# Kernel optimization log

Hardware: AMD Instinct MI355X
Metric: run time of the kernel (lower is better)

The kernel has to match this reference:

```python
import jax, jax.numpy as jnp
import numpy as np

B, T, C = 4, 2048, 1024
H = 16
DH = C // H  # 64


def setup_inputs() -> dict:
    key = jax.random.key(0)
    ks = jax.random.split(key, 10)
    s_in = 1.0 / np.sqrt(C)
    x = jax.random.normal(ks[0], (B, T, C), dtype=jnp.float32)
    # stacked per-head projection weights: [H, C, DH]
    Wq = jax.random.normal(ks[1], (H, C, DH), dtype=jnp.float32) * s_in
    bq = jnp.zeros((H, DH), dtype=jnp.float32)
    Wk = jax.random.normal(ks[2], (H, C, DH), dtype=jnp.float32) * s_in
    bk = jnp.zeros((H, DH), dtype=jnp.float32)
    Wv = jax.random.normal(ks[3], (H, C, DH), dtype=jnp.float32) * s_in
    bv = jnp.zeros((H, DH), dtype=jnp.float32)
    Wo = jax.random.normal(ks[4], (C, C), dtype=jnp.float32) * s_in
    bo = jnp.zeros((C,), dtype=jnp.float32)
    return {"x": x, "Wq": Wq, "bq": bq, "Wk": Wk, "bk": bk,
            "Wv": Wv, "bv": bv, "Wo": Wo, "bo": bo}


def reference(x, Wq, bq, Wk, bk, Wv, bv, Wo, bo):
    # per-head projections: (B,T,C) x (H,C,DH) -> (B,H,T,DH)
    q = jnp.einsum('btc,hcd->bhtd', x, Wq) + bq[None, :, None, :]
    k = jnp.einsum('btc,hcd->bhtd', x, Wk) + bk[None, :, None, :]
    v = jnp.einsum('btc,hcd->bhtd', x, Wv) + bv[None, :, None, :]
    # scores scaled by C**-0.5 (C = full input embedding dim, as in source)
    scale = jnp.float32(C) ** -0.5
    scores = jnp.einsum('bhtd,bhsd->bhts', q, k) * scale  # (B,H,T,T)
    causal = jnp.tril(jnp.ones((T, T), dtype=bool))
    scores = jnp.where(causal, scores, -jnp.inf)
    attn = jax.nn.softmax(scores, axis=-1)
    out = jnp.einsum('bhts,bhsd->bhtd', attn, v)  # (B,H,T,DH)
    out = out.transpose(0, 2, 1, 3).reshape(B, T, C)  # concat heads
    return out @ Wo + bo
```

## Files before the change

### kernel.cpp

```cpp
#include <hip/hip_runtime.h>
#include <hip/hip_bf16.h>

#define TDIM 2048
#define BDIM 4
#define CDIM 1024
#define HDIM 16
#define DH   64

typedef __hip_bfloat16 bf16;
typedef __attribute__((ext_vector_type(8))) short bf16x8;
typedef __attribute__((ext_vector_type(4))) short bf16x4;
typedef __attribute__((ext_vector_type(4))) float f32x4;

__device__ __forceinline__ void async_ld16(const bf16* g, bf16* l) {
    __builtin_amdgcn_global_load_lds(
        (const __attribute__((address_space(1))) unsigned int*)g,
        (__attribute__((address_space(3))) unsigned int*)l, 16, 0, 0);
}

__device__ __forceinline__ unsigned short bf16bits(float x) {
    bf16 b = __float2bfloat16(x);
    return *(unsigned short*)&b;
}

__device__ __forceinline__ float fast_exp2(float x) {
#if __has_builtin(__builtin_amdgcn_exp2f)
    return __builtin_amdgcn_exp2f(x);
#else
    return exp2f(x);
#endif
}

__device__ __forceinline__ f32x4 mfma_16x16x16_bf16(bf16x4 a, bf16x4 b, f32x4 c) {
#if __has_builtin(__builtin_amdgcn_mfma_f32_16x16x16_bf16)
    return __builtin_amdgcn_mfma_f32_16x16x16_bf16(a, b, c, 0, 0, 0);
#elif __has_builtin(__builtin_amdgcn_mfma_f32_16x16x16bf16_1k)
    return __builtin_amdgcn_mfma_f32_16x16x16bf16_1k(a, b, c, 0, 0, 0);
#else
    asm volatile("v_mfma_f32_16x16x16_bf16 %0, %1, %2, %0"
                 : "+v"(c) : "v"(a), "v"(b));
    return c;
#endif
}

__global__ void convert_x4(const float4* __restrict__ src, ushort4* __restrict__ dst, int n4) {
    int i = blockIdx.x * blockDim.x + threadIdx.x;
    if (i >= n4) return;
    float4 v = src[i];
    ushort4 o;
    o.x = bf16bits(v.x); o.y = bf16bits(v.y);
    o.z = bf16bits(v.z); o.w = bf16bits(v.w);
    dst[i] = o;
}

__global__ void convert_biases(const float* __restrict__ b0, const float* __restrict__ b1,
                               const float* __restrict__ b2, const float* __restrict__ b3,
                               bf16* __restrict__ dst) {
    int i = blockIdx.x * blockDim.x + threadIdx.x;
    int which = i >> 10, j = i & 1023;
    const float* src = (which == 0) ? b0 : (which == 1) ? b1 : (which == 2) ? b2 : b3;
    dst[i] = __float2bfloat16(src[j]);
}

__global__ __launch_bounds__(256) void transpose_qkv_kernel(
    const float* __restrict__ Wq, const float* __restrict__ Wk, const float* __restrict__ Wv,
    bf16* __restrict__ WqT, bf16* __restrict__ WkT, bf16* __restrict__ WvT) {
    __shared__ float tile[64][65];
    const int which = blockIdx.z >> 4, h = blockIdx.z & 15;
    const float* W  = ((which == 0) ? Wq  : (which == 1) ? Wk  : Wv)  + (size_t)h * CDIM * DH;
    bf16*        WT = ((which == 0) ? WqT : (which == 1) ? WkT : WvT) + (size_t)h * CDIM * DH;
    const int c0 = blockIdx.x * 64;
    for (int it = 0; it < 16; it++) {
        int e = it * 256 + threadIdx.x;
        int r = e >> 6, col = e & 63;
        tile[r][col] = W[(size_t)(c0 + r) * DH + col];
    }
    __syncthreads();
    for (int it = 0; it < 16; it++) {
        int e = it * 256 + threadIdx.x;
        int r = e >> 6, col = e & 63;
        WT[(size_t)r * CDIM + c0 + col] = __float2bfloat16(tile[col][r]);
    }
}

__global__ __launch_bounds__(256) void transpose_wo_kernel(
    const float* __restrict__ W, bf16* __restrict__ WT) {
    __shared__ float tile[64][65];
    const int c0 = blockIdx.x * 64, d0 = blockIdx.y * 64;
    for (int it = 0; it < 16; it++) {
        int e = it * 256 + threadIdx.x;
        int r = e >> 6, col = e & 63;
        tile[r][col] = W[(size_t)(c0 + r) * CDIM + d0 + col];
    }
    __syncthreads();
    for (int it = 0; it < 16; it++) {
        int e = it * 256 + threadIdx.x;
        int r = e >> 6, col = e & 63;
        WT[(size_t)(d0 + r) * CDIM + c0 + col] = __float2bfloat16(tile[col][r]);
    }
}

__global__ __launch_bounds__(256) void transpose_v_kernel(
    const bf16* __restrict__ V, bf16* __restrict__ Vt) {
    __shared__ unsigned short tile[64][65];
    const int bh = blockIdx.y, t0 = blockIdx.x * 64;
    const unsigned short* Vp  = (const unsigned short*)V + ((size_t)bh * TDIM + t0) * DH;
    unsigned short*       Vtp = (unsigned short*)Vt + (size_t)bh * DH * TDIM;
    for (int it = 0; it < 16; it++) {
        int e = it * 256 + threadIdx.x;
        int r = e >> 6, c = e & 63;
        tile[r][c] = Vp[(size_t)r * DH + c];
    }
    __syncthreads();
    for (int it = 0; it < 16; it++) {
        int e = it * 256 + threadIdx.x;
        int r = e >> 6, c = e & 63;
        Vtp[(size_t)r * TDIM + t0 + c] = tile[c][r];
    }
}

__global__ __launch_bounds__(256) void proj_qkv_kernel(
    const bf16* __restrict__ X,
    const bf16* __restrict__ WqT, const bf16* __restrict__ WkT, const bf16* __restrict__ WvT,
    const bf16* __restrict__ bq,  const bf16* __restrict__ bk,  const bf16* __restrict__ bvv,
    bf16* __restrict__ Qo, bf16* __restrict__ Ko, bf16* __restrict__ Vo)
{
    const int z = blockIdx.z;
    const bf16* Bt   = (z == 0) ? WqT : (z == 1) ? WkT : WvT;
    const bf16* bias = (z == 0) ? bq  : (z == 1) ? bk  : bvv;

    __shared__ __align__(16) bf16 As[128 * 32];
    __shared__ __align__(16) bf16 Bs[128 * 32];

    const int tid  = threadIdx.x;
    const int lane = tid & 63;
    const int wave = tid >> 6;
    const int wr = wave >> 1, wc = wave & 1;
    const int l15 = lane & 15, quad = lane >> 4;

    const int blockM = blockIdx.y * 128;
    const int blockN = blockIdx.x * 128;

    f32x4 acc[4][4];
    for (int i = 0; i < 4; i++)
        for (int j = 0; j < 4; j++)
            acc[i][j] = (f32x4){0.f, 0.f, 0.f, 0.f};

    const int srow = lane >> 2, scol = (lane & 3) * 8;
    for (int k0 = 0; k0 < CDIM; k0 += 32) {
        for (int cc = 0; cc < 2; cc++) {
            int chunk = wave * 2 + cc;
            int row = chunk * 16 + srow;
            async_ld16(&X [(size_t)(blockM + row) * CDIM + k0 + scol], &As[chunk * 512]);
            async_ld16(&Bt[(size_t)(blockN + row) * CDIM + k0 + scol], &Bs[chunk * 512]);
        }
        __syncthreads();

        bf16x8 af[4], bfr[4];
        for (int mi = 0; mi < 4; mi++)
            af[mi] = *(const bf16x8*)&As[(wr * 64 + mi * 16 + l15) * 32 + quad * 8];
        for (int ni = 0; ni < 4; ni++)
            bfr[ni] = *(const bf16x8*)&Bs[(wc * 64 + ni * 16 + l15) * 32 + quad * 8];

        for (int mi = 0; mi < 4; mi++)
            for (int ni = 0; ni < 4; ni++)
                acc[mi][ni] = __builtin_amdgcn_mfma_f32_16x16x32_bf16(
                    af[mi], bfr[ni], acc[mi][ni], 0, 0, 0);
        __syncthreads();
    }

    for (int mi = 0; mi < 4; mi++) {
        int mbase = blockM + wr * 64 + mi * 16 + quad * 4;
        for (int ni = 0; ni < 4; ni++) {
            int n = blockN + wc * 64 + ni * 16 + l15;
            float bval = __bfloat162float(bias[n]);
            int h = n >> 6, d = n & 63;
            for (int r = 0; r < 4; r++) {
                int mm = mbase + r;
                int b = mm >> 11, t = mm & 2047;
                float val = acc[mi][ni][r] + bval;
                size_t idx = (((size_t)b * HDIM + h) * TDIM + t) * DH + d;
                if (z == 0)      Qo[idx] = __float2bfloat16(val * 0.045084439f);
                else if (z == 1) Ko[idx] = __float2bfloat16(val);
                else             Vo[idx] = __float2bfloat16(val);
            }
        }
    }
}

__global__ __launch_bounds__(256) void proj_out_kernel(
    const bf16* __restrict__ X, const bf16* __restrict__ Bt,
    const bf16* __restrict__ bias, float* __restrict__ Out)
{
    __shared__ __align__(16) bf16 As[128 * 32];
    __shared__ __align__(16) bf16 Bs[128 * 32];

    const int tid  = threadIdx.x;
    const int lane = tid & 63;
    const int wave = tid >> 6;
    const int wr = wave >> 1, wc = wave & 1;
    const int l15 = lane & 15, quad = lane >> 4;

    const int blockM = blockIdx.y * 128;
    const int blockN = blockIdx.x * 128;

    f32x4 acc[4][4];
    for (int i = 0; i < 4; i++)
        for (int j = 0; j < 4; j++)
            acc[i][j] = (f32x4){0.f, 0.f, 0.f, 0.f};

    const int srow = lane >> 2, scol = (lane & 3) * 8;
    for (int k0 = 0; k0 < CDIM; k0 += 32) {
        for (int cc = 0; cc < 2; cc++) {
            int chunk = wave * 2 + cc;
            int row = chunk * 16 + srow;
            async_ld16(&X [(size_t)(blockM + row) * CDIM + k0 + scol], &As[chunk * 512]);
            async_ld16(&Bt[(size_t)(blockN + row) * CDIM + k0 + scol], &Bs[chunk * 512]);
        }
        __syncthreads();

        bf16x8 af[4], bfr[4];
        for (int mi = 0; mi < 4; mi++)
            af[mi] = *(const bf16x8*)&As[(wr * 64 + mi * 16 + l15) * 32 + quad * 8];
        for (int ni = 0; ni < 4; ni++)
            bfr[ni] = *(const bf16x8*)&Bs[(wc * 64 + ni * 16 + l15) * 32 + quad * 8];

        for (int mi = 0; mi < 4; mi++)
            for (int ni = 0; ni < 4; ni++)
                acc[mi][ni] = __builtin_amdgcn_mfma_f32_16x16x32_bf16(
                    af[mi], bfr[ni], acc[mi][ni], 0, 0, 0);
        __syncthreads();
    }

    for (int mi = 0; mi < 4; mi++) {
        int mbase = blockM + wr * 64 + mi * 16 + quad * 4;
        for (int ni = 0; ni < 4; ni++) {
            int n = blockN + wc * 64 + ni * 16 + l15;
            float bval = __bfloat162float(bias[n]);
            for (int r = 0; r < 4; r++)
                Out[(size_t)(mbase + r) * CDIM + n] = acc[mi][ni][r] + bval;
        }
    }
}

__global__ __launch_bounds__(256, 4) void attn_kernel(
    const bf16* __restrict__ Q, const bf16* __restrict__ Kb,
    const bf16* __restrict__ Vt, bf16* __restrict__ Y)
{
    const int bh    = blockIdx.y;
    const int qT    = (int)gridDim.x - 1 - blockIdx.x;
    const int qBase = qT * 64;
    const int tid  = threadIdx.x;
    const int lane = tid & 63, wave = tid >> 6;
    const int l15 = lane & 15, quad = lane >> 4;

    __shared__ __align__(16) bf16 smem[3 * 2 * 64 * 64];

    const size_t qrow = (size_t)bh * TDIM + qBase + wave * 16 + l15;
    const bf16x8 qf0 = *(const bf16x8*)&Q[qrow * DH + quad * 8];
    const bf16x8 qf1 = *(const bf16x8*)&Q[qrow * DH + 32 + quad * 8];

    f32x4 o[4];
    for (int mt = 0; mt < 4; mt++) o[mt] = (f32x4){0.f, 0.f, 0.f, 0.f};
    float lsum = 0.f;

    const int srow = (wave << 4) + (lane >> 3);
    const int ssc  = (((lane & 7) ^ (lane >> 3)) << 3);
    const bf16* kSrc0 = Kb + ((size_t)bh * TDIM + srow) * DH + ssc;
    const bf16* vSrc0 = Vt + ((size_t)bh * DH + srow) * TDIM + ssc;

    const int swA   = l15 & 7;
    const int kcol0 = ((quad ^ swA) << 3);
    const int kcol1 = (((4 + quad) ^ swA) << 3);
    const int u2    = quad >> 1, intra = ((quad & 1) << 2);

    const int nkt  = qT + 1;
    const int qloc = wave * 16 + l15;

    bf16* kD0 = smem + (wave * 16) * 64;
    bf16* vD0 = smem + 4096 + (wave * 16) * 64;

#define STAGE(tile, buf)                                            \
    do {                                                            \
        const bf16* kS_ = kSrc0 + (size_t)(tile) * 64 * DH;         \
        const bf16* vS_ = vSrc0 + (size_t)(tile) * 64;              \
        bf16* kD_ = kD0 + (buf) * 8192;                             \
        bf16* vD_ = vD0 + (buf) * 8192;                             \
        async_ld16(kS_,            kD_);                            \
        async_ld16(kS_ + 8 * DH,   kD_ + 8 * 64);                   \
        async_ld16(vS_,            vD_);                            \
        async_ld16(vS_ + 8 * TDIM, vD_ + 8 * 64);                   \
    } while (0)

    STAGE(0, 0);
    if (nkt > 1) {
        STAGE(1, 1);
        asm volatile("s_waitcnt vmcnt(4)" ::: "memory");
    } else {
        asm volatile("s_waitcnt vmcnt(0)" ::: "memory");
    }
    __builtin_amdgcn_s_barrier();

    int cb = 0;
    for (int kt = 0; kt < nkt; kt++) {
        if (kt + 2 < nkt) {
            int pb = cb + 2; if (pb >= 3) pb -= 3;
            STAGE(kt + 2, pb);
        }

        const bf16* Ks = smem + cb * 8192;
        const bf16* Vs = Ks + 4096;

        const bool diag = (kt == qT);
        for (int nt = 0; nt < 4; nt++) {
            bf16x8 kf0 = *(const bf16x8*)&Ks[(nt * 16 + l15) * 64 + kcol0];
            bf16x8 kf1 = *(const bf16x8*)&Ks[(nt * 16 + l15) * 64 + kcol1];
            bf16x4 vA[4];
            for (int mt = 0; mt < 4; mt++)
                vA[mt] = *(const bf16x4*)&Vs[(mt * 16 + l15) * 64 +
                                             (((nt * 2 + u2) ^ swA) << 3) + intra];

            f32x4 s = (f32x4){0.f, 0.f, 0.f, 0.f};
            s = __builtin_amdgcn_mfma_f32_16x16x32_bf16(kf0, qf0, s, 0, 0, 0);
            s = __builtin_amdgcn_mfma_f32_16x16x32_bf16(kf1, qf1, s, 0, 0, 0);

            bf16x4 pb16;
            for (int r = 0; r < 4; r++) {
                float pe = fast_exp2(s[r]);
                if (diag && (nt * 16 + quad * 4 + r > qloc)) pe = 0.f;
                lsum += pe;
                pb16[r] = (short)bf16bits(pe);
            }
            for (int mt = 0; mt < 4; mt++)
                o[mt] = mfma_16x16x16_bf16(vA[mt], pb16, o[mt]);
        }

        if (kt + 1 < nkt) {
            if (kt + 2 < nkt) asm volatile("s_waitcnt vmcnt(4)" ::: "memory");
            else              asm volatile("s_waitcnt vmcnt(0)" ::: "memory");
            __builtin_amdgcn_s_barrier();
        }
        cb = (cb == 2) ? 0 : cb + 1;
    }
#undef STAGE

    __syncthreads();

    float v = lsum;
    v += __shfl_xor(v, 16, 64);
    v += __shfl_xor(v, 32, 64);
    const float inv = 1.0f / v;

    unsigned short* sm = (unsigned short*)smem;
    for (int mt = 0; mt < 4; mt++) {
        unsigned short pk[4];
        for (int r = 0; r < 4; r++) pk[r] = bf16bits(o[mt][r] * inv);
        *(ushort4*)&sm[(wave * 16 + l15) * 72 + mt * 16 + quad * 4] = *(ushort4*)pk;
    }
    const int b = bh >> 4, h = bh & 15;
    const int qq = lane >> 2, part = lane & 3;
    const int t = qBase + wave * 16 + qq;
    uint4 c0 = *(const uint4*)&sm[(wave * 16 + qq) * 72 + part * 16];
    uint4 c1 = *(const uint4*)&sm[(wave * 16 + qq) * 72 + part * 16 + 8];
    *(uint4*)&Y[((size_t)b * TDIM + t) * CDIM + h * DH + part * 16]     = c0;
    *(uint4*)&Y[((size_t)b * TDIM + t) * CDIM + h * DH + part * 16 + 8] = c1;
}

extern "C" void kernel_launch(void* const* d_in, const int* in_sizes, int n_in,
                              void* d_out, int out_size, void* d_ws, size_t ws_size,
                              hipStream_t stream) {
    (void)in_sizes; (void)n_in; (void)out_size; (void)ws_size;

    char* ws = (char*)d_ws;
    const size_t SZ_BHTD = (size_t)BDIM * HDIM * TDIM * DH * sizeof(bf16);
    const size_t SZ_W    = (size_t)HDIM * CDIM * DH * sizeof(bf16);
    bf16* Qb  = (bf16*)(ws);
    bf16* Kb  = (bf16*)(ws + SZ_BHTD);
    bf16* Vt  = (bf16*)(ws + 2 * SZ_BHTD);
    bf16* Y   = (bf16*)(ws + 3 * SZ_BHTD);
    bf16* WqT = (bf16*)(ws + 4 * SZ_BHTD);
    bf16* WkT = (bf16*)(ws + 4 * SZ_BHTD + SZ_W);
    bf16* WvT = (bf16*)(ws + 4 * SZ_BHTD + 2 * SZ_W);
    bf16* WoT = (bf16*)(ws + 4 * SZ_BHTD + 3 * SZ_W);
    bf16* xC  = (bf16*)(ws + 4 * SZ_BHTD + 4 * SZ_W);
    bf16* bqC = (bf16*)(ws + 5 * SZ_BHTD + 4 * SZ_W);
    bf16* bkC = bqC + 1024;
    bf16* bvC = bqC + 2048;
    bf16* boC = bqC + 3072;
    bf16* Vb  = (bf16*)d_out;

    const int nX4 = (BDIM * TDIM * CDIM) / 4;
    convert_x4<<<nX4 / 256, 256, 0, stream>>>((const float4*)d_in[0], (ushort4*)xC, nX4);
    convert_biases<<<16, 256, 0, stream>>>((const float*)d_in[2], (const float*)d_in[4],
                                           (const float*)d_in[6], (const float*)d_in[8], bqC);

    transpose_qkv_kernel<<<dim3(CDIM / 64, 1, 48), 256, 0, stream>>>(
        (const float*)d_in[1], (const float*)d_in[3], (const float*)d_in[5], WqT, WkT, WvT);
    transpose_wo_kernel<<<dim3(CDIM / 64, CDIM / 64), 256, 0, stream>>>(
        (const float*)d_in[7], WoT);

    dim3 gq(CDIM / 128, (BDIM * TDIM) / 128, 3);
    proj_qkv_kernel<<<gq, 256, 0, stream>>>(xC, WqT, WkT, WvT, bqC, bkC, bvC, Qb, Kb, Vb);

    transpose_v_kernel<<<dim3(TDIM / 64, BDIM * HDIM), 256, 0, stream>>>(Vb, Vt);

    attn_kernel<<<dim3(TDIM / 64, BDIM * HDIM), 256, 0, stream>>>(Qb, Kb, Vt, Y);

    proj_out_kernel<<<dim3(CDIM / 128, (BDIM * TDIM) / 128), 256, 0, stream>>>(
        Y, WoT, boC, (float*)d_out);
}
```

Before: 316.2 us.

## Process two 64-row query groups per attention block to reuse K/V tiles

Each attention block now handles 128 query rows as two groups of 64, so every K/V tile staged into shared memory serves both groups and global K/V traffic is halved. The pipeline drops from a triple-buffered async scheme with partial vmcnt waits to double buffering with a full __syncthreads each iteration. The cost is more registers for accumulators, half as many blocks (less parallelism and coarser causal load balance), and possibly less overlap of loads with compute.

```diff
diff --git a/kernel.cpp b/kernel.cpp
--- a/kernel.cpp
+++ b/kernel.cpp
@@ -249,20 +249,25 @@
 {
     const int bh    = blockIdx.y;
     const int qT    = (int)gridDim.x - 1 - blockIdx.x;
-    const int qBase = qT * 64;
+    const int qBase = qT * 128;
     const int tid  = threadIdx.x;
     const int lane = tid & 63, wave = tid >> 6;
     const int l15 = lane & 15, quad = lane >> 4;
 
-    __shared__ __align__(16) bf16 smem[3 * 2 * 64 * 64];
-
-    const size_t qrow = (size_t)bh * TDIM + qBase + wave * 16 + l15;
-    const bf16x8 qf0 = *(const bf16x8*)&Q[qrow * DH + quad * 8];
-    const bf16x8 qf1 = *(const bf16x8*)&Q[qrow * DH + 32 + quad * 8];
-
-    f32x4 o[4];
-    for (int mt = 0; mt < 4; mt++) o[mt] = (f32x4){0.f, 0.f, 0.f, 0.f};
-    float lsum = 0.f;
+    __shared__ __align__(16) bf16 smem[2 * 2 * 64 * 64];
+
+    bf16x8 qf[2][2];
+    for (int g = 0; g < 2; g++) {
+        const size_t qrow = (size_t)bh * TDIM + qBase + g * 64 + wave * 16 + l15;
+        qf[g][0] = *(const bf16x8*)&Q[qrow * DH + quad * 8];
+        qf[g][1] = *(const bf16x8*)&Q[qrow * DH + 32 + quad * 8];
+    }
+
+    f32x4 o[2][4];
+    for (int g = 0; g < 2; g++)
+        for (int mt = 0; mt < 4; mt++)
+            o[g][mt] = (f32x4){0.f, 0.f, 0.f, 0.f};
+    float lsum[2] = {0.f, 0.f};
 
     const int srow = (wave << 4) + (lane >> 3);
     const int ssc  = (((lane & 7) ^ (lane >> 3)) << 3);
@@ -274,7 +279,7 @@
     const int kcol1 = (((4 + quad) ^ swA) << 3);
     const int u2    = quad >> 1, intra = ((quad & 1) << 2);
 
-    const int nkt  = qT + 1;
+    const int nkt  = 2 * qT + 2;
     const int qloc = wave * 16 + l15;
 
     bf16* kD0 = smem + (wave * 16) * 64;
@@ -293,25 +298,15 @@
     } while (0)
 
     STAGE(0, 0);
-    if (nkt > 1) {
-        STAGE(1, 1);
-        asm volatile("s_waitcnt vmcnt(4)" ::: "memory");
-    } else {
-        asm volatile("s_waitcnt vmcnt(0)" ::: "memory");
-    }
-    __builtin_amdgcn_s_barrier();
-
-    int cb = 0;
+    __syncthreads();
+
+    int cur = 0;
     for (int kt = 0; kt < nkt; kt++) {
-        if (kt + 2 < nkt) {
-            int pb = cb + 2; if (pb >= 3) pb -= 3;
-            STAGE(kt + 2, pb);
-        }
-
-        const bf16* Ks = smem + cb * 8192;
+        if (kt + 1 < nkt) STAGE(kt + 1, cur ^ 1);
+        const bf16* Ks = smem + cur * 8192;
         const bf16* Vs = Ks + 4096;
 
-        const bool diag = (kt == qT);
+        const int dg = kt - 2 * qT;
         for (int nt = 0; nt < 4; nt++) {
             bf16x8 kf0 = *(const bf16x8*)&Ks[(nt * 16 + l15) * 64 + kcol0];
             bf16x8 kf1 = *(const bf16x8*)&Ks[(nt * 16 + l15) * 64 + kcol1];
@@ -320,50 +315,49 @@
                 vA[mt] = *(const bf16x4*)&Vs[(mt * 16 + l15) * 64 +
                                              (((nt * 2 + u2) ^ swA) << 3) + intra];
 
-            f32x4 s = (f32x4){0.f, 0.f, 0.f, 0.f};
-            s = __builtin_amdgcn_mfma_f32_16x16x32_bf16(kf0, qf0, s, 0, 0, 0);
-            s = __builtin_amdgcn_mfma_f32_16x16x32_bf16(kf1, qf1, s, 0, 0, 0);
-
-            bf16x4 pb16;
-            for (int r = 0; r < 4; r++) {
-                float pe = fast_exp2(s[r]);
-                if (diag && (nt * 16 + quad * 4 + r > qloc)) pe = 0.f;
-                lsum += pe;
-                pb16[r] = (short)bf16bits(pe);
+            for (int g = 0; g < 2; g++) {
+                if (dg == 1 && g == 0) continue;
+                f32x4 s = (f32x4){0.f, 0.f, 0.f, 0.f};
+                s = __builtin_amdgcn_mfma_f32_16x16x32_bf16(kf0, qf[g][0], s, 0, 0, 0);
+                s = __builtin_amdgcn_mfma_f32_16x16x32_bf16(kf1, qf[g][1], s, 0, 0, 0);
+
+                const bool diag = (dg == g);
+                bf16x4 pb;
+                for (int r = 0; r < 4; r++) {
+                    float pe = fast_exp2(s[r]);
+                    if (diag && (nt * 16 + quad * 4 + r > qloc)) pe = 0.f;
+                    lsum[g] += pe;
+                    pb[r] = (short)bf16bits(pe);
+                }
+                for (int mt = 0; mt < 4; mt++)
+                    o[g][mt] = mfma_16x16x16_bf16(vA[mt], pb, o[g][mt]);
             }
-            for (int mt = 0; mt < 4; mt++)
-                o[mt] = mfma_16x16x16_bf16(vA[mt], pb16, o[mt]);
-        }
-
-        if (kt + 1 < nkt) {
-            if (kt + 2 < nkt) asm volatile("s_waitcnt vmcnt(4)" ::: "memory");
-            else              asm volatile("s_waitcnt vmcnt(0)" ::: "memory");
-            __builtin_amdgcn_s_barrier();
-        }
-        cb = (cb == 2) ? 0 : cb + 1;
+        }
+        __syncthreads();
+        cur ^= 1;
     }
 #undef STAGE
 
-    __syncthreads();
-
-    float v = lsum;
-    v += __shfl_xor(v, 16, 64);
-    v += __shfl_xor(v, 32, 64);
-    const float inv = 1.0f / v;
-
+    const int b = bh >> 4, h = bh & 15;
     unsigned short* sm = (unsigned short*)smem;
-    for (int mt = 0; mt < 4; mt++) {
-        unsigned short pk[4];
-        for (int r = 0; r < 4; r++) pk[r] = bf16bits(o[mt][r] * inv);
-        *(ushort4*)&sm[(wave * 16 + l15) * 72 + mt * 16 + quad * 4] = *(ushort4*)pk;
-    }
-    const int b = bh >> 4, h = bh & 15;
-    const int qq = lane >> 2, part = lane & 3;
-    const int t = qBase + wave * 16 + qq;
-    uint4 c0 = *(const uint4*)&sm[(wave * 16 + qq) * 72 + part * 16];
-    uint4 c1 = *(const uint4*)&sm[(wave * 16 + qq) * 72 + part * 16 + 8];
-    *(uint4*)&Y[((size_t)b * TDIM + t) * CDIM + h * DH + part * 16]     = c0;
-    *(uint4*)&Y[((size_t)b * TDIM + t) * CDIM + h * DH + part * 16 + 8] = c1;
+    for (int g = 0; g < 2; g++) {
+        float v = lsum[g];
+        v += __shfl_xor(v, 16, 64);
+        v += __shfl_xor(v, 32, 64);
+        const float inv = 1.0f / v;
+
+        for (int mt = 0; mt < 4; mt++) {
+            unsigned short pk[4];
+            for (int r = 0; r < 4; r++) pk[r] = bf16bits(o[g][mt][r] * inv);
+            *(ushort4*)&sm[(wave * 16 + l15) * 72 + mt * 16 + quad * 4] = *(ushort4*)pk;
+        }
+        const int qq = lane >> 2, part = lane & 3;
+        const int t = qBase + g * 64 + wave * 16 + qq;
+        uint4 c0 = *(const uint4*)&sm[(wave * 16 + qq) * 72 + part * 16];
+        uint4 c1 = *(const uint4*)&sm[(wave * 16 + qq) * 72 + part * 16 + 8];
+        *(uint4*)&Y[((size_t)b * TDIM + t) * CDIM + h * DH + part * 16]     = c0;
+        *(uint4*)&Y[((size_t)b * TDIM + t) * CDIM + h * DH + part * 16 + 8] = c1;
+    }
 }
 
 extern "C" void kernel_launch(void* const* d_in, const int* in_sizes, int n_in,
@@ -404,7 +398,7 @@
 
     transpose_v_kernel<<<dim3(TDIM / 64, BDIM * HDIM), 256, 0, stream>>>(Vb, Vt);
 
-    attn_kernel<<<dim3(TDIM / 64, BDIM * HDIM), 256, 0, stream>>>(Qb, Kb, Vt, Y);
+    attn_kernel<<<dim3(TDIM / 128, BDIM * HDIM), 256, 0, stream>>>(Qb, Kb, Vt, Y);
 
     proj_out_kernel<<<dim3(CDIM / 128, (BDIM * TDIM) / 128), 256, 0, stream>>>(
         Y, WoT, boC, (float*)d_out);
```

Result: faster. 296.6 us (-6.2%).
